# Performance work log

Measured on AMD Instinct MI355X. Metric: run time of the kernel, lower is better.

Reference implementation:

```python
import jax, jax.numpy as jnp
import numpy as np

WIDTH = 128
N_NODE = 1024
N_REL = 12
OPS = ["Copy", "And", "Or", "Chaining", "Not"]


def setup_inputs() -> dict:
    key = jax.random.key(0)
    k1, k2, k3, k4, k5, k6 = jax.random.split(key, 6)
    return {
        "inputs": jax.random.uniform(k1, (WIDTH, N_NODE), dtype=jnp.float32),
        "database": jax.random.uniform(k2, (N_REL, N_NODE, N_NODE), dtype=jnp.float32),
        "arg1_weights": jax.random.normal(k3, (WIDTH, WIDTH), dtype=jnp.float32),
        "arg2_weights": jax.random.normal(k4, (WIDTH, WIDTH), dtype=jnp.float32),
        "op_weights": jax.random.normal(k5, (WIDTH, len(OPS)), dtype=jnp.float32),
        "chain_weights": jax.random.normal(k6, (WIDTH, 2 * N_REL), dtype=jnp.float32),
    }


def _chain(x, database, chain_weights):
    # x: [width, n_node], database: [n_rel, n, n], chain_weights: [width, 2*n_rel]
    n_rel = database.shape[0]
    cw = jax.nn.softmax(chain_weights, axis=1)
    w_fwd, w_bwd = cw[:, :n_rel], cw[:, n_rel:]  # [width, n_rel] each
    # Per-width relation-averaged adjacency: A[w,a,b] = sum_r D[r,a,b]*w_fwd[w,r] + D[r,b,a]*w_bwd[w,r]
    avg_rel = (jnp.einsum('rab,wr->wab', database, w_fwd)
               + jnp.einsum('rba,wr->wab', database, w_bwd))
    chained = jnp.einsum('wa,wab->wb', x, avg_rel)  # [width, n_node]
    return 1.0 - jnp.exp(-chained)


def reference(inputs, database, arg1_weights, arg2_weights, op_weights, chain_weights):
    # inputs: [width, n_node] fuzzy truth values
    arg1 = jax.nn.softmax(arg1_weights, axis=0).T @ inputs  # [width, n_node]
    arg2 = jax.nn.softmax(arg2_weights, axis=0).T @ inputs
    opw = jax.nn.softmax(op_weights, axis=1).T  # [n_ops, width]

    out = jnp.zeros_like(inputs)
    for i, op in enumerate(OPS):
        if op == 'Copy':
            res = arg2
        elif op == 'And':
            res = arg1 * arg2
        elif op == 'Or':
            res = arg1 + arg2 - arg1 * arg2
        elif op == 'Chaining':
            res = _chain(arg2, database, chain_weights)
        elif op == 'Not':
            res = 1.0 - arg1
        out = out + res * opw[i][:, None]
    return out
```

## Files before the change

kernel.cpp:

```cpp
#include <hip/hip_runtime.h>
#include <math.h>

#define W128  128
#define NNODE 1024
#define NREL  12
#define TS    72

#define OFF_ARG1  0
#define OFF_ARG2  131072
#define OFF_ARG2B 262144
#define OFF_PART  327680

typedef short bf16x8 __attribute__((ext_vector_type(8)));
typedef short short4v __attribute__((ext_vector_type(4)));
typedef float f32x4  __attribute__((ext_vector_type(4)));

__device__ __forceinline__ short bf16t(float x) {
    return (short)(__float_as_uint(x) >> 16);
}
__device__ __forceinline__ float bf16f(short s) {
    return __uint_as_float((unsigned)(unsigned short)s << 16);
}
__device__ __forceinline__ unsigned pk2(float lo, float hi) {
    return (__float_as_uint(hi) & 0xFFFF0000u) | (__float_as_uint(lo) >> 16);
}

__global__ __launch_bounds__(512) void k_args3(const float* __restrict__ inputs,
                                               const float* __restrict__ a1w,
                                               const float* __restrict__ a2w,
                                               float* __restrict__ ws,
                                               short* __restrict__ x2b) {
    __shared__ __align__(16) char smem[33280];
    float* lin = (float*)smem;
    float* sm1 = (float*)(smem + 16896);
    float* sm2 = sm1 + 16 * W128;
    int t = threadIdx.x;
    int bid = blockIdx.x;
    int n0 = (bid & 31) * 32;
    int w0 = (bid >> 5) * 16;
#pragma unroll
    for (int u = 0; u < 8; ++u) {
        int idx = t + u * 512;
        int j = idx >> 5, nn = idx & 31;
        lin[j * 33 + nn] = inputs[j * NNODE + n0 + nn];
    }
    {
        int c = t >> 4, i = t & 15;
        const float* src = (c < 16) ? a1w : a2w;
        float* dst = (c < 16) ? sm1 : sm2;
        int w_loc = c & 15;
        int wcol = w0 + w_loc;
        float v[8]; float mx = -1e30f;
#pragma unroll
        for (int k = 0; k < 8; ++k) {
            v[k] = src[(i * 8 + k) * W128 + wcol];
            mx = fmaxf(mx, v[k]);
        }
#pragma unroll
        for (int off = 8; off; off >>= 1) mx = fmaxf(mx, __shfl_xor(mx, off));
        float s = 0.f;
#pragma unroll
        for (int k = 0; k < 8; ++k) { v[k] = expf(v[k] - mx); s += v[k]; }
#pragma unroll
        for (int off = 8; off; off >>= 1) s += __shfl_xor(s, off);
        float inv = 1.0f / s;
#pragma unroll
        for (int k = 0; k < 8; ++k) dst[w_loc * W128 + i * 8 + k] = v[k] * inv;
    }
    __syncthreads();
    int nn = t & 31, w_loc = t >> 5;
    int n = n0 + nn, w = w0 + w_loc;
    const float* s1 = sm1 + w_loc * W128;
    const float* s2 = sm2 + w_loc * W128;
    float a1 = 0.f, a2 = 0.f;
#pragma unroll 4
    for (int j = 0; j < W128; ++j) {
        float in = lin[j * 33 + nn];
        a1 = fmaf(s1[j], in, a1);
        a2 = fmaf(s2[j], in, a2);
    }
    ws[OFF_ARG1 + w * NNODE + n] = a1;
    ws[OFF_ARG2 + w * NNODE + n] = a2;
    x2b[w * NNODE + n] = bf16t(a2);
}

__global__ __launch_bounds__(512) void k_chain4(const float* __restrict__ db,
                                                const float* __restrict__ chw,
                                                const short* __restrict__ x2b,
                                                short* __restrict__ partF,
                                                short* __restrict__ partB) {
    __shared__ __align__(16) short Tf[64 * TS];
    __shared__ __align__(16) short Tt[64 * TS];
    __shared__ float wfs[W128 * NREL];
    __shared__ float wbs[W128 * NREL];

    int tid = threadIdx.x;
    int B0  = blockIdx.x * 64;
    int A0  = blockIdx.y * 64;

    int a0 = 2 * (tid >> 4), c0 = 4 * (tid & 15);
    const float* gbase = db + (size_t)(A0 + a0) * NNODE + B0 + c0;
    const size_t rstep = (size_t)NNODE * NNODE;
    float4 g0 = *(const float4*)(gbase);
    float4 g1 = *(const float4*)(gbase + NNODE);

    if (tid < 128) {
        float u[24]; float mx = -1e30f;
        for (int k = 0; k < 24; ++k) { u[k] = chw[tid * 24 + k]; mx = fmaxf(mx, u[k]); }
        float s = 0.f;
        for (int k = 0; k < 24; ++k) { u[k] = expf(u[k] - mx); s += u[k]; }
        float inv = 1.0f / s;
        for (int k = 0; k < 12; ++k) wfs[tid * NREL + k] = u[k] * inv;
        for (int k = 0; k < 12; ++k) wbs[tid * NREL + k] = u[12 + k] * inv;
    }

    int l   = tid & 63, wid = tid >> 6;
    int wm  = wid >> 2;
    int wn  = wid & 3;
    int l16 = l & 15, lq = l >> 4;

    bf16x8 bfF[2][2], bfB[2][2];
#pragma unroll
    for (int ni = 0; ni < 2; ++ni)
#pragma unroll
        for (int ks = 0; ks < 2; ++ks) {
            int w = wn * 32 + ni * 16 + l16;
            bfF[ni][ks] = *(const bf16x8*)&x2b[w * NNODE + A0 + ks * 32 + lq * 8];
            bfB[ni][ks] = *(const bf16x8*)&x2b[w * NNODE + B0 + ks * 32 + lq * 8];
        }

    f32x4 accF[2][2], accB[2][2];
#pragma unroll
    for (int mi = 0; mi < 2; ++mi)
#pragma unroll
        for (int ni = 0; ni < 2; ++ni) {
            accF[mi][ni] = (f32x4){0.f, 0.f, 0.f, 0.f};
            accB[mi][ni] = (f32x4){0.f, 0.f, 0.f, 0.f};
        }

#pragma unroll 2
    for (int r = 0; r < NREL; ++r) {
        uint2 p0 = {pk2(g0.x, g0.y), pk2(g0.z, g0.w)};
        uint2 p1 = {pk2(g1.x, g1.y), pk2(g1.z, g1.w)};
        *(uint2*)&Tf[a0 * TS + c0]       = p0;
        *(uint2*)&Tf[(a0 + 1) * TS + c0] = p1;
        *(unsigned*)&Tt[(c0 + 0) * TS + a0] = pk2(g0.x, g1.x);
        *(unsigned*)&Tt[(c0 + 1) * TS + a0] = pk2(g0.y, g1.y);
        *(unsigned*)&Tt[(c0 + 2) * TS + a0] = pk2(g0.z, g1.z);
        *(unsigned*)&Tt[(c0 + 3) * TS + a0] = pk2(g0.w, g1.w);
        __syncthreads();

        float4 n0v = g0, n1v = g1;
        if (r + 1 < NREL) {
            const float* g = gbase + (size_t)(r + 1) * rstep;
            n0v = *(const float4*)(g);
            n1v = *(const float4*)(g + NNODE);
        }

        f32x4 tF[2][2], tB[2][2];
#pragma unroll
        for (int mi = 0; mi < 2; ++mi)
#pragma unroll
            for (int ni = 0; ni < 2; ++ni) {
                tF[mi][ni] = (f32x4){0.f, 0.f, 0.f, 0.f};
                tB[mi][ni] = (f32x4){0.f, 0.f, 0.f, 0.f};
            }

#pragma unroll
        for (int ks = 0; ks < 2; ++ks) {
            bf16x8 AF[2], AB[2];
#pragma unroll
            for (int mi = 0; mi < 2; ++mi) {
                int row = wm * 32 + mi * 16 + l16;
                int off = ks * 32 + lq * 8;
                AF[mi] = *(const bf16x8*)&Tt[row * TS + off];
                AB[mi] = *(const bf16x8*)&Tf[row * TS + off];
            }
#pragma unroll
            for (int mi = 0; mi < 2; ++mi)
#pragma unroll
                for (int ni = 0; ni < 2; ++ni) {
                    tF[mi][ni] = __builtin_amdgcn_mfma_f32_16x16x32_bf16(
                        AF[mi], bfF[ni][ks], tF[mi][ni], 0, 0, 0);
                    tB[mi][ni] = __builtin_amdgcn_mfma_f32_16x16x32_bf16(
                        AB[mi], bfB[ni][ks], tB[mi][ni], 0, 0, 0);
                }
        }
        __syncthreads();

#pragma unroll
        for (int ni = 0; ni < 2; ++ni) {
            int w = wn * 32 + ni * 16 + l16;
            float wfv = wfs[w * NREL + r];
            float wbv = wbs[w * NREL + r];
#pragma unroll
            for (int mi = 0; mi < 2; ++mi)
#pragma unroll
                for (int v = 0; v < 4; ++v) {
                    accF[mi][ni][v] += wfv * tF[mi][ni][v];
                    accB[mi][ni][v] += wbv * tB[mi][ni][v];
                }
        }
        g0 = n0v; g1 = n1v;
    }

#pragma unroll
    for (int mi = 0; mi < 2; ++mi)
#pragma unroll
        for (int v = 0; v < 4; ++v) {
            int m = wm * 32 + mi * 16 + lq * 4 + v;
#pragma unroll
            for (int ni = 0; ni < 2; ++ni) {
                int w = wn * 32 + ni * 16 + l16;
                partF[(size_t)blockIdx.y * (NNODE * W128) + (B0 + m) * W128 + w]
                    = bf16t(accF[mi][ni][v]);
                partB[(size_t)blockIdx.x * (NNODE * W128) + (A0 + m) * W128 + w]
                    = bf16t(accB[mi][ni][v]);
            }
        }
}

__global__ __launch_bounds__(256) void k_reduce4(const float* __restrict__ ws,
                                                 const float* __restrict__ opww,
                                                 const short* __restrict__ partF,
                                                 const short* __restrict__ partB,
                                                 float* __restrict__ out) {
    __shared__ float chs[64 * 17];
    int t = threadIdx.x;
    int n0 = blockIdx.x * 64;
    int w0 = blockIdx.y * 16;
    {
        int n_loc = t >> 2;
        int wq = (t & 3) * 4;
        size_t base = (size_t)(n0 + n_loc) * W128 + w0 + wq;
        float c0 = 0.f, c1 = 0.f, c2 = 0.f, c3 = 0.f;
#pragma unroll
        for (int s = 0; s < 16; ++s) {
            short4v pf = *(const short4v*)&partF[(size_t)s * (NNODE * W128) + base];
            short4v pb = *(const short4v*)&partB[(size_t)s * (NNODE * W128) + base];
            c0 += bf16f(pf[0]) + bf16f(pb[0]);
            c1 += bf16f(pf[1]) + bf16f(pb[1]);
            c2 += bf16f(pf[2]) + bf16f(pb[2]);
            c3 += bf16f(pf[3]) + bf16f(pb[3]);
        }
        chs[n_loc * 17 + wq + 0] = c0;
        chs[n_loc * 17 + wq + 1] = c1;
        chs[n_loc * 17 + wq + 2] = c2;
        chs[n_loc * 17 + wq + 3] = c3;
    }
    __syncthreads();
    {
        int w_loc = t >> 4;
        int n4 = (t & 15) * 4;
        int w = w0 + w_loc;
        float ch[4];
#pragma unroll
        for (int j = 0; j < 4; ++j) ch[j] = chs[(n4 + j) * 17 + w_loc];
        float v[5], mx = -1e30f;
#pragma unroll
        for (int k = 0; k < 5; ++k) { v[k] = opww[w * 5 + k]; mx = fmaxf(mx, v[k]); }
        float s5 = 0.f;
#pragma unroll
        for (int k = 0; k < 5; ++k) { v[k] = expf(v[k] - mx); s5 += v[k]; }
        float inv = 1.0f / s5;
        float4 a1 = *(const float4*)&ws[OFF_ARG1 + w * NNODE + n0 + n4];
        float4 a2 = *(const float4*)&ws[OFF_ARG2 + w * NNODE + n0 + n4];
        float a1v[4] = {a1.x, a1.y, a1.z, a1.w};
        float a2v[4] = {a2.x, a2.y, a2.z, a2.w};
        float ov[4];
#pragma unroll
        for (int j = 0; j < 4; ++j) {
            float p = a1v[j] * a2v[j];
            ov[j] = inv * (v[0] * a2v[j] + v[1] * p + v[2] * (a1v[j] + a2v[j] - p)
                  + v[3] * (1.0f - expf(-ch[j])) + v[4] * (1.0f - a1v[j]));
        }
        float4 o = {ov[0], ov[1], ov[2], ov[3]};
        *(float4*)&out[w * NNODE + n0 + n4] = o;
    }
}

extern "C" void kernel_launch(void* const* d_in, const int* in_sizes, int n_in,
                              void* d_out, int out_size, void* d_ws, size_t ws_size,
                              hipStream_t stream) {
    const float* inputs = (const float*)d_in[0];
    const float* db     = (const float*)d_in[1];
    const float* a1w    = (const float*)d_in[2];
    const float* a2w    = (const float*)d_in[3];
    const float* opww   = (const float*)d_in[4];
    const float* chw    = (const float*)d_in[5];
    float* ws  = (float*)d_ws;
    float* out = (float*)d_out;
    short* x2b   = (short*)(ws + OFF_ARG2B);
    short* partF = (short*)(ws + OFF_PART);
    short* partB = partF + (size_t)16 * NNODE * W128;

    hipLaunchKernelGGL(k_args3, dim3(256), dim3(512), 0, stream,
                       inputs, a1w, a2w, ws, x2b);
    hipLaunchKernelGGL(k_chain4, dim3(16, 16), dim3(512), 0, stream,
                       db, chw, x2b, partF, partB);
    hipLaunchKernelGGL(k_reduce4, dim3(16, 8), dim3(256), 0, stream,
                       ws, opww, partF, partB, out);
}
```

Before: 33.97 us.

## Fuse arg projections into chain and reduce kernels, removing the args launch

Removes the separate k_args3 kernel. Each chain block now recomputes its own bf16 arg2 slice for its A and B columns with MFMA from the inputs and the softmaxed arg2 weights, holding it in shared memory. The reduce kernel recomputes arg1 and arg2 in fp32 for its tile before combining. This drops one launch and the global round trip for the arg buffers, at the cost of redundant projection work in every block and much larger shared memory use, which may lower occupancy.

```diff
diff --git a/kernel.cpp b/kernel.cpp
--- a/kernel.cpp
+++ b/kernel.cpp
@@ -5,11 +5,7 @@
 #define NNODE 1024
 #define NREL  12
 #define TS    72
-
-#define OFF_ARG1  0
-#define OFF_ARG2  131072
-#define OFF_ARG2B 262144
-#define OFF_PART  327680
+#define XS    136
 
 typedef short bf16x8 __attribute__((ext_vector_type(8)));
 typedef short short4v __attribute__((ext_vector_type(4)));
@@ -25,78 +21,26 @@
     return (__float_as_uint(hi) & 0xFFFF0000u) | (__float_as_uint(lo) >> 16);
 }
 
-__global__ __launch_bounds__(512) void k_args3(const float* __restrict__ inputs,
-                                               const float* __restrict__ a1w,
-                                               const float* __restrict__ a2w,
-                                               float* __restrict__ ws,
-                                               short* __restrict__ x2b) {
-    __shared__ __align__(16) char smem[33280];
-    float* lin = (float*)smem;
-    float* sm1 = (float*)(smem + 16896);
-    float* sm2 = sm1 + 16 * W128;
-    int t = threadIdx.x;
-    int bid = blockIdx.x;
-    int n0 = (bid & 31) * 32;
-    int w0 = (bid >> 5) * 16;
-#pragma unroll
-    for (int u = 0; u < 8; ++u) {
-        int idx = t + u * 512;
-        int j = idx >> 5, nn = idx & 31;
-        lin[j * 33 + nn] = inputs[j * NNODE + n0 + nn];
-    }
-    {
-        int c = t >> 4, i = t & 15;
-        const float* src = (c < 16) ? a1w : a2w;
-        float* dst = (c < 16) ? sm1 : sm2;
-        int w_loc = c & 15;
-        int wcol = w0 + w_loc;
-        float v[8]; float mx = -1e30f;
-#pragma unroll
-        for (int k = 0; k < 8; ++k) {
-            v[k] = src[(i * 8 + k) * W128 + wcol];
-            mx = fmaxf(mx, v[k]);
-        }
-#pragma unroll
-        for (int off = 8; off; off >>= 1) mx = fmaxf(mx, __shfl_xor(mx, off));
-        float s = 0.f;
-#pragma unroll
-        for (int k = 0; k < 8; ++k) { v[k] = expf(v[k] - mx); s += v[k]; }
-#pragma unroll
-        for (int off = 8; off; off >>= 1) s += __shfl_xor(s, off);
-        float inv = 1.0f / s;
-#pragma unroll
-        for (int k = 0; k < 8; ++k) dst[w_loc * W128 + i * 8 + k] = v[k] * inv;
-    }
-    __syncthreads();
-    int nn = t & 31, w_loc = t >> 5;
-    int n = n0 + nn, w = w0 + w_loc;
-    const float* s1 = sm1 + w_loc * W128;
-    const float* s2 = sm2 + w_loc * W128;
-    float a1 = 0.f, a2 = 0.f;
-#pragma unroll 4
-    for (int j = 0; j < W128; ++j) {
-        float in = lin[j * 33 + nn];
-        a1 = fmaf(s1[j], in, a1);
-        a2 = fmaf(s2[j], in, a2);
-    }
-    ws[OFF_ARG1 + w * NNODE + n] = a1;
-    ws[OFF_ARG2 + w * NNODE + n] = a2;
-    x2b[w * NNODE + n] = bf16t(a2);
-}
-
-__global__ __launch_bounds__(512) void k_chain4(const float* __restrict__ db,
+__global__ __launch_bounds__(512) void k_chainA(const float* __restrict__ db,
+                                                const float* __restrict__ inputs,
+                                                const float* __restrict__ a2w,
                                                 const float* __restrict__ chw,
-                                                const short* __restrict__ x2b,
                                                 short* __restrict__ partF,
                                                 short* __restrict__ partB) {
-    __shared__ __align__(16) short Tf[64 * TS];
-    __shared__ __align__(16) short Tt[64 * TS];
-    __shared__ float wfs[W128 * NREL];
-    __shared__ float wbs[W128 * NREL];
+    __shared__ __align__(16) char smem[65536];
+    short* smT = (short*)smem;
+    short* X   = (short*)smem;
+    short* inT = (short*)(smem + 34816);
+    short* Tf  = (short*)(smem + 34816);
+    short* Tt  = (short*)(smem + 44032);
+    float* wfs = (float*)(smem + 53248);
+    float* wbs = (float*)(smem + 59392);
 
     int tid = threadIdx.x;
-    int B0  = blockIdx.x * 64;
-    int A0  = blockIdx.y * 64;
+    int gx = blockIdx.x, gy = blockIdx.y;
+    int B0 = gx * 64, A0 = gy * 64;
+    int l = tid & 63, wid = tid >> 6;
+    int l16 = l & 15, lq = l >> 4;
 
     int a0 = 2 * (tid >> 4), c0 = 4 * (tid & 15);
     const float* gbase = db + (size_t)(A0 + a0) * NNODE + B0 + c0;
@@ -104,29 +48,95 @@
     float4 g0 = *(const float4*)(gbase);
     float4 g1 = *(const float4*)(gbase + NNODE);
 
+    {
+        int i = tid & 15, cb = tid >> 4;
+#pragma unroll
+        for (int p = 0; p < 4; ++p) {
+            int c = p * 32 + cb;
+            float v[8]; float mx = -1e30f;
+#pragma unroll
+            for (int k = 0; k < 8; ++k) { v[k] = a2w[(i * 8 + k) * W128 + c]; mx = fmaxf(mx, v[k]); }
+#pragma unroll
+            for (int off = 8; off; off >>= 1) mx = fmaxf(mx, __shfl_xor(mx, off));
+            float s = 0.f;
+#pragma unroll
+            for (int k = 0; k < 8; ++k) { v[k] = expf(v[k] - mx); s += v[k]; }
+#pragma unroll
+            for (int off = 8; off; off >>= 1) s += __shfl_xor(s, off);
+            float inv = 1.0f / s;
+            int4 pkv;
+            pkv.x = (int)pk2(v[0] * inv, v[1] * inv);
+            pkv.y = (int)pk2(v[2] * inv, v[3] * inv);
+            pkv.z = (int)pk2(v[4] * inv, v[5] * inv);
+            pkv.w = (int)pk2(v[6] * inv, v[7] * inv);
+            *(int4*)&smT[c * XS + i * 8] = pkv;
+        }
+    }
+
+    f32x4 xacc[8];
+#pragma unroll
+    for (int ni = 0; ni < 8; ++ni) xacc[ni] = (f32x4){0.f, 0.f, 0.f, 0.f};
+
+#pragma unroll
+    for (int half = 0; half < 2; ++half) {
+#pragma unroll
+        for (int u = 0; u < 2; ++u) {
+            int slot = tid + u * 512;
+            int jp = slot >> 5;
+            int cg = slot & 31;
+            int j = half * 64 + 2 * jp;
+            int gcol = (cg < 16) ? (A0 + cg * 4) : (B0 + (cg - 16) * 4);
+            float4 r0 = *(const float4*)&inputs[(size_t)j * NNODE + gcol];
+            float4 r1 = *(const float4*)&inputs[(size_t)(j + 1) * NNODE + gcol];
+            int nb = cg * 4;
+            *(unsigned*)&inT[(nb + 0) * TS + 2 * jp] = pk2(r0.x, r1.x);
+            *(unsigned*)&inT[(nb + 1) * TS + 2 * jp] = pk2(r0.y, r1.y);
+            *(unsigned*)&inT[(nb + 2) * TS + 2 * jp] = pk2(r0.z, r1.z);
+            *(unsigned*)&inT[(nb + 3) * TS + 2 * jp] = pk2(r0.w, r1.w);
+        }
+        __syncthreads();
+#pragma unroll
+        for (int kh = 0; kh < 2; ++kh) {
+            int kk = half * 2 + kh;
+            bf16x8 Af = *(const bf16x8*)&inT[(wid * 16 + l16) * TS + kh * 32 + lq * 8];
+#pragma unroll
+            for (int ni = 0; ni < 8; ++ni) {
+                bf16x8 Bf = *(const bf16x8*)&smT[(ni * 16 + l16) * XS + kk * 32 + lq * 8];
+                xacc[ni] = __builtin_amdgcn_mfma_f32_16x16x32_bf16(Af, Bf, xacc[ni], 0, 0, 0);
+            }
+        }
+        __syncthreads();
+    }
+
+#pragma unroll
+    for (int ni = 0; ni < 8; ++ni) {
+        int w = ni * 16 + l16;
+        int nb = wid * 16 + lq * 4;
+        uint2 pv;
+        pv.x = pk2(xacc[ni][0], xacc[ni][1]);
+        pv.y = pk2(xacc[ni][2], xacc[ni][3]);
+        *(uint2*)&X[w * XS + nb] = pv;
+    }
     if (tid < 128) {
-        float u[24]; float mx = -1e30f;
-        for (int k = 0; k < 24; ++k) { u[k] = chw[tid * 24 + k]; mx = fmaxf(mx, u[k]); }
+        float u2[24]; float mx = -1e30f;
+        for (int k = 0; k < 24; ++k) { u2[k] = chw[tid * 24 + k]; mx = fmaxf(mx, u2[k]); }
         float s = 0.f;
-        for (int k = 0; k < 24; ++k) { u[k] = expf(u[k] - mx); s += u[k]; }
+        for (int k = 0; k < 24; ++k) { u2[k] = expf(u2[k] - mx); s += u2[k]; }
         float inv = 1.0f / s;
-        for (int k = 0; k < 12; ++k) wfs[tid * NREL + k] = u[k] * inv;
-        for (int k = 0; k < 12; ++k) wbs[tid * NREL + k] = u[12 + k] * inv;
-    }
-
-    int l   = tid & 63, wid = tid >> 6;
-    int wm  = wid >> 2;
-    int wn  = wid & 3;
-    int l16 = l & 15, lq = l >> 4;
-
+        for (int k = 0; k < 12; ++k) wfs[tid * NREL + k] = u2[k] * inv;
+        for (int k = 0; k < 12; ++k) wbs[tid * NREL + k] = u2[12 + k] * inv;
+    }
+    __syncthreads();
+
+    int wm = wid >> 2, wn = wid & 3;
     bf16x8 bfF[2][2], bfB[2][2];
 #pragma unroll
     for (int ni = 0; ni < 2; ++ni)
 #pragma unroll
         for (int ks = 0; ks < 2; ++ks) {
             int w = wn * 32 + ni * 16 + l16;
-            bfF[ni][ks] = *(const bf16x8*)&x2b[w * NNODE + A0 + ks * 32 + lq * 8];
-            bfB[ni][ks] = *(const bf16x8*)&x2b[w * NNODE + B0 + ks * 32 + lq * 8];
+            bfF[ni][ks] = *(const bf16x8*)&X[w * XS + ks * 32 + lq * 8];
+            bfB[ni][ks] = *(const bf16x8*)&X[w * XS + 64 + ks * 32 + lq * 8];
         }
 
     f32x4 accF[2][2], accB[2][2];
@@ -212,26 +222,80 @@
 #pragma unroll
             for (int ni = 0; ni < 2; ++ni) {
                 int w = wn * 32 + ni * 16 + l16;
-                partF[(size_t)blockIdx.y * (NNODE * W128) + (B0 + m) * W128 + w]
+                partF[(size_t)gy * (NNODE * W128) + (B0 + m) * W128 + w]
                     = bf16t(accF[mi][ni][v]);
-                partB[(size_t)blockIdx.x * (NNODE * W128) + (A0 + m) * W128 + w]
+                partB[(size_t)gx * (NNODE * W128) + (A0 + m) * W128 + w]
                     = bf16t(accB[mi][ni][v]);
             }
         }
 }
 
-__global__ __launch_bounds__(256) void k_reduce4(const float* __restrict__ ws,
-                                                 const float* __restrict__ opww,
-                                                 const short* __restrict__ partF,
-                                                 const short* __restrict__ partB,
-                                                 float* __restrict__ out) {
-    __shared__ float chs[64 * 17];
+__global__ __launch_bounds__(256) void k_redB(const float* __restrict__ inputs,
+                                              const float* __restrict__ a1w,
+                                              const float* __restrict__ a2w,
+                                              const float* __restrict__ opww,
+                                              const short* __restrict__ partF,
+                                              const short* __restrict__ partB,
+                                              float* __restrict__ out) {
+    __shared__ __align__(16) char smem[62720];
+    float* lin = (float*)smem;
+    float* sm1 = (float*)(smem + 33280);
+    float* sm2 = (float*)(smem + 41472);
+    float* a1s = (float*)(smem + 49664);
+    float* a2s = (float*)(smem + 54016);
+    float* chs = (float*)(smem + 58368);
     int t = threadIdx.x;
     int n0 = blockIdx.x * 64;
     int w0 = blockIdx.y * 16;
+
+#pragma unroll
+    for (int u = 0; u < 32; ++u) {
+        int idx = t + u * 256;
+        int j = idx >> 6, nn = idx & 63;
+        lin[j * 65 + nn] = inputs[(size_t)j * NNODE + n0 + nn];
+    }
     {
-        int n_loc = t >> 2;
-        int wq = (t & 3) * 4;
+        int i = t & 15, c = t >> 4;
+#pragma unroll
+        for (int m2 = 0; m2 < 2; ++m2) {
+            const float* src = m2 ? a2w : a1w;
+            float* dst = m2 ? sm2 : sm1;
+            int wcol = w0 + c;
+            float v[8]; float mx = -1e30f;
+#pragma unroll
+            for (int k = 0; k < 8; ++k) { v[k] = src[(i * 8 + k) * W128 + wcol]; mx = fmaxf(mx, v[k]); }
+#pragma unroll
+            for (int off = 8; off; off >>= 1) mx = fmaxf(mx, __shfl_xor(mx, off));
+            float s = 0.f;
+#pragma unroll
+            for (int k = 0; k < 8; ++k) { v[k] = expf(v[k] - mx); s += v[k]; }
+#pragma unroll
+            for (int off = 8; off; off >>= 1) s += __shfl_xor(s, off);
+            float inv = 1.0f / s;
+#pragma unroll
+            for (int k = 0; k < 8; ++k) dst[c * W128 + i * 8 + k] = v[k] * inv;
+        }
+    }
+    __syncthreads();
+#pragma unroll
+    for (int u = 0; u < 4; ++u) {
+        int pair = t + u * 256;
+        int nn = pair & 63, w_loc = pair >> 6;
+        const float* s1 = sm1 + w_loc * W128;
+        const float* s2 = sm2 + w_loc * W128;
+        float a1 = 0.f, a2 = 0.f;
+#pragma unroll 4
+        for (int j = 0; j < W128; ++j) {
+            float in = lin[j * 65 + nn];
+            a1 = fmaf(s1[j], in, a1);
+            a2 = fmaf(s2[j], in, a2);
+        }
+        a1s[w_loc * 68 + nn] = a1;
+        a2s[w_loc * 68 + nn] = a2;
+    }
+    __syncthreads();
+    {
+        int n_loc = t >> 2, wq = (t & 3) * 4;
         size_t base = (size_t)(n0 + n_loc) * W128 + w0 + wq;
         float c0 = 0.f, c1 = 0.f, c2 = 0.f, c3 = 0.f;
 #pragma unroll
@@ -250,12 +314,8 @@
     }
     __syncthreads();
     {
-        int w_loc = t >> 4;
-        int n4 = (t & 15) * 4;
+        int w_loc = t >> 4, n4 = (t & 15) * 4;
         int w = w0 + w_loc;
-        float ch[4];
-#pragma unroll
-        for (int j = 0; j < 4; ++j) ch[j] = chs[(n4 + j) * 17 + w_loc];
         float v[5], mx = -1e30f;
 #pragma unroll
         for (int k = 0; k < 5; ++k) { v[k] = opww[w * 5 + k]; mx = fmaxf(mx, v[k]); }
@@ -263,19 +323,18 @@
 #pragma unroll
         for (int k = 0; k < 5; ++k) { v[k] = expf(v[k] - mx); s5 += v[k]; }
         float inv = 1.0f / s5;
-        float4 a1 = *(const float4*)&ws[OFF_ARG1 + w * NNODE + n0 + n4];
-        float4 a2 = *(const float4*)&ws[OFF_ARG2 + w * NNODE + n0 + n4];
-        float a1v[4] = {a1.x, a1.y, a1.z, a1.w};
-        float a2v[4] = {a2.x, a2.y, a2.z, a2.w};
         float ov[4];
 #pragma unroll
         for (int j = 0; j < 4; ++j) {
-            float p = a1v[j] * a2v[j];
-            ov[j] = inv * (v[0] * a2v[j] + v[1] * p + v[2] * (a1v[j] + a2v[j] - p)
-                  + v[3] * (1.0f - expf(-ch[j])) + v[4] * (1.0f - a1v[j]));
+            float ch = chs[(n4 + j) * 17 + w_loc];
+            float a1 = a1s[w_loc * 68 + n4 + j];
+            float a2 = a2s[w_loc * 68 + n4 + j];
+            float p = a1 * a2;
+            ov[j] = inv * (v[0] * a2 + v[1] * p + v[2] * (a1 + a2 - p)
+                  + v[3] * (1.0f - expf(-ch)) + v[4] * (1.0f - a1));
         }
         float4 o = {ov[0], ov[1], ov[2], ov[3]};
-        *(float4*)&out[w * NNODE + n0 + n4] = o;
+        *(float4*)&out[(size_t)w * NNODE + n0 + n4] = o;
     }
 }
 
@@ -288,16 +347,12 @@
     const float* a2w    = (const float*)d_in[3];
     const float* opww   = (const float*)d_in[4];
     const float* chw    = (const float*)d_in[5];
-    float* ws  = (float*)d_ws;
     float* out = (float*)d_out;
-    short* x2b   = (short*)(ws + OFF_ARG2B);
-    short* partF = (short*)(ws + OFF_PART);
+    short* partF = (short*)d_ws;
     short* partB = partF + (size_t)16 * NNODE * W128;
 
-    hipLaunchKernelGGL(k_args3, dim3(256), dim3(512), 0, stream,
-                       inputs, a1w, a2w, ws, x2b);
-    hipLaunchKernelGGL(k_chain4, dim3(16, 16), dim3(512), 0, stream,
-                       db, chw, x2b, partF, partB);
-    hipLaunchKernelGGL(k_reduce4, dim3(16, 8), dim3(256), 0, stream,
-                       ws, opww, partF, partB, out);
-}
+    hipLaunchKernelGGL(k_chainA, dim3(16, 16), dim3(512), 0, stream,
+                       db, inputs, a2w, chw, partF, partB);
+    hipLaunchKernelGGL(k_redB, dim3(16, 8), dim3(256), 0, stream,
+                       inputs, a1w, a2w, opww, partF, partB, out);
+}
```

Result: slower. 48.86 us (+43.8%).
